# Performance work log

Measured on AMD Instinct MI355X. Metric: run time of the kernel, lower is better.

## Reference

```python
import jax, jax.numpy as jnp
import numpy as np

APREC = 8   # activation fractional bits
PPREC = 8   # parameter fractional bits
IWIDTH = 3  # integer width -> clamp to [-2**IWIDTH, 2**IWIDTH - 1]

QMAX = 2.0 ** IWIDTH - 1.0
QMIN = -(2.0 ** IWIDTH)


def quant(v, prec):
    # round to 2**-prec grid (torch.round and jnp.round both round-half-to-even)
    s = 2.0 ** prec
    return jnp.round(v * s) / s


def round_max(v):
    # the relu-chain in the source is exactly a clamp to [QMIN, QMAX]
    return jnp.clip(v, QMIN, QMAX)


def fixed_point_conv(x, w, b):
    """Quantized 'conv': each elementwise product w[j,m,p,q]*x[b,m,k+p,l+q] is
    rounded to the activation grid and clamped BEFORE summation, then bias added.
    x: [B,Cin,H,W], w: [Cout,Cin,K,K], b: [Cout].
    Loop is over the KxK fixed kernel offsets (25), fully vectorized over B/Cout/Cin/space."""
    w = quant(w, PPREC)
    b = quant(b, PPREC)
    K = w.shape[2]
    Ho = x.shape[2] - K + 1
    Wo = x.shape[3] - K + 1
    out = jnp.zeros((x.shape[0], w.shape[0], Ho, Wo), dtype=x.dtype)
    for p in range(K):
        for q in range(K):
            # [B, Cout, Cin, Ho, Wo]
            prod = x[:, None, :, p:p + Ho, q:q + Wo] * w[None, :, :, p, q, None, None]
            prod = round_max(quant(prod, APREC))
            out = out + prod.sum(axis=2)
    return out + b[None, :, None, None]


def fixed_point_fc(x, w, b):
    # x: [B, in], w: [out, in], b: [out]
    w = round_max(quant(w, PPREC))
    b = round_max(quant(b, PPREC))
    x = round_max(quant(x, APREC))
    out = x @ w.T + b[None, :]
    out = round_max(out)
    return quant(out, APREC)


def max_pool2(x):
    return jax.lax.reduce_window(x, -jnp.inf, jax.lax.max,
                                 (1, 1, 2, 2), (1, 1, 2, 2), 'VALID')


def setup_inputs() -> dict:
    key = jax.random.key(0)
    ks = jax.random.split(key, 9)
    B = 2048
    return {
        'x': jax.random.normal(ks[0], (B, 1, 28, 28), jnp.float32),
        'conv1_w': jax.random.normal(ks[1], (10, 1, 5, 5), jnp.float32) * 0.2,
        'conv1_b': jax.random.normal(ks[2], (10,), jnp.float32) * 0.1,
        'conv2_w': jax.random.normal(ks[3], (20, 10, 5, 5), jnp.float32) * 0.1,
        'conv2_b': jax.random.normal(ks[4], (20,), jnp.float32) * 0.1,
        'fc1_w': jax.random.normal(ks[5], (50, 320), jnp.float32) * 0.05,
        'fc1_b': jax.random.normal(ks[6], (50,), jnp.float32) * 0.05,
        'fc2_w': jax.random.normal(ks[7], (10, 50), jnp.float32) * 0.1,
        'fc2_b': jax.random.normal(ks[8], (10,), jnp.float32) * 0.1,
    }


def reference(x, conv1_w, conv1_b, conv2_w, conv2_b, fc1_w, fc1_b, fc2_w, fc2_b):
    x = quant(x, APREC)
    conv1_input = x
    x = fixed_point_conv(x, conv1_w, conv1_b)          # [B,10,24,24]
    x = quant(x, APREC)
    conv1_output = x
    x = jax.nn.relu(max_pool2(x))                      # [B,10,12,12]
    x = quant(x, APREC)
    conv2_input = x
    x = fixed_point_conv(x, conv2_w, conv2_b)          # [B,20,8,8]
    x = quant(x, APREC)
    conv2_output = x
    # Dropout2d / F.dropout are identity in eval mode
    x = jax.nn.relu(max_pool2(x))                      # [B,20,4,4]
    x = x.reshape(-1, 320)
    x = quant(x, APREC)
    fc1_input = x
    x = fixed_point_fc(x, fc1_w, fc1_b)                # [B,50]
    x = quant(x, APREC)
    fc1_output = x
    x = jax.nn.relu(x)
    x = quant(x, APREC)
    fc2_input = x
    x = fixed_point_fc(x, fc2_w, fc2_b)                # [B,10]
    x = quant(x, APREC)
    fc2_output = x
    logp = jax.nn.log_softmax(x, axis=1)
    return (logp, conv1_input, conv1_output, conv2_input, conv2_output,
            fc1_input, fc1_output, fc2_input, fc2_output)
```

## Files before the change

kernel.cpp:

```cpp
#include <hip/hip_runtime.h>
#include <math.h>


#define NB 2048

#define OFF_LOGP   0
#define OFF_C1IN   (OFF_LOGP  + NB*10)
#define OFF_C1OUT  (OFF_C1IN  + NB*784)
#define OFF_C2IN   (OFF_C1OUT + NB*5760)
#define OFF_C2OUT  (OFF_C2IN  + NB*1440)
#define OFF_FC1IN  (OFF_C2OUT + NB*1280)
#define OFF_FC1OUT (OFF_FC1IN + NB*320)
#define OFF_FC2IN  (OFF_FC1OUT+ NB*50)
#define OFF_FC2OUT (OFF_FC2IN + NB*50)

#define MAGIC_F 12582912.0f

#define WS_WT1 0
#define WS_B1  20480
#define WS_WT2 20544
#define WS_B2  21344
#define WS_CW2 21360
#define WS_CB2 26960
#define WS_CW1 26980
#define WS_CB1 27260

__device__ __forceinline__ float clamp8(float v) {
    return __builtin_amdgcn_fmed3f(v, -8.0f, 7.0f);
}

__global__ __launch_bounds__(256)
void k0_prep(const float* __restrict__ cw1, const float* __restrict__ cb1,
             const float* __restrict__ cw2, const float* __restrict__ cb2,
             const float* __restrict__ fw1, const float* __restrict__ fb1,
             const float* __restrict__ fw2, const float* __restrict__ fb2,
             float* __restrict__ ws)
{
    const int t = threadIdx.x, b = blockIdx.x;
    if (b < 50) {
        const float* src = fw1 + b * 320;
        for (int i = t; i < 320; i += 256)
            ws[WS_WT1 + i * 64 + b] = clamp8(rintf(src[i] * 256.0f) * (1.0f / 256.0f));
    } else if (b == 50) {
        for (int idx = t; idx < 320 * 14; idx += 256) {
            int i = idx / 14, j = 50 + idx % 14;
            ws[WS_WT1 + i * 64 + j] = 0.0f;
        }
        for (int idx = t; idx < 800; idx += 256) {
            int k = idx >> 4, j = idx & 15;
            ws[WS_WT2 + idx] = (j < 10) ? clamp8(rintf(fw2[j * 50 + k] * 256.0f) * (1.0f / 256.0f)) : 0.0f;
        }
        if (t < 64) ws[WS_B1 + t] = (t < 50) ? clamp8(rintf(fb1[t] * 256.0f) * (1.0f / 256.0f)) : 0.0f;
        if (t < 16) ws[WS_B2 + t] = (t < 10) ? clamp8(rintf(fb2[t] * 256.0f) * (1.0f / 256.0f)) : 0.0f;
    } else {
        for (int idx = t; idx < 5600; idx += 256) {
            int cc = idx / 28, col = idx % 28;
            ws[WS_CW2 + idx] = (col < 25) ? rintf(cw2[cc * 25 + col] * 256.0f) : 0.0f;
        }
        if (t < 20) ws[WS_CB2 + t] = rintf(cb2[t] * 256.0f);
        for (int idx = t; idx < 280; idx += 256) {
            int cc = idx / 28, col = idx % 28;
            ws[WS_CW1 + idx] = (col < 25) ? rintf(cw1[cc * 25 + col] * 256.0f) : 0.0f;
        }
        if (t >= 32 && t < 42) ws[WS_CB1 + (t - 32)] = rintf(cb1[t - 32] * 256.0f);
    }
}

__global__ __launch_bounds__(256, 2)
void k12w(const float* __restrict__ x, const float* __restrict__ ws,
          float* __restrict__ out)
{
    __shared__ __align__(16) float s_w1[280];
    __shared__ float s_b1[10];
    __shared__ __align__(16) float s_w2[5600];
    __shared__ float s_b2[20];
    __shared__ __align__(16) float s_x[4][784];
    __shared__ __align__(16) float s_p1[4][1440];

    const int t    = threadIdx.x;
    const int img0 = blockIdx.x * 4;

    {
        const float4* wsrc = (const float4*)(ws + WS_CW2);
        float4* wdst = (float4*)s_w2;
        for (int i = t; i < 1400; i += 256) wdst[i] = wsrc[i];
        if (t < 70) ((float4*)s_w1)[t] = ((const float4*)(ws + WS_CW1))[t];
    }
    if (t >= 70 && t < 80)  s_b1[t - 70] = ws[WS_CB1 + (t - 70)];
    if (t >= 80 && t < 100) s_b2[t - 80] = ws[WS_CB2 + (t - 80)];

    {
        const float* xg = x + (size_t)img0 * 784;
        float* c1in_g = out + OFF_C1IN + (size_t)img0 * 784;
        float* sxf = &s_x[0][0];
        for (int i = t; i < 3136; i += 256) {
            float v = rintf(xg[i] * 256.0f) * (1.0f / 256.0f);
            sxf[i] = v;
            c1in_g[i] = v;
        }
    }
    __syncthreads();

    const int wv  = t >> 6;
    const int L   = t & 63;
    const int img = img0 + wv;
    const float* sx = s_x[wv];
    float*       sp = s_p1[wv];
    float*       sf = s_x[wv];

    if (L < 48) {
        const int i  = L >> 1;
        const int jh = L & 1;

        for (int co = 0; co < 10; co++) {
            asm volatile("" ::: "memory");
            float wreg[28];
            {
                const float* wb = s_w1 + co * 28;
                #pragma unroll
                for (int k = 0; k < 7; k++) {
                    float4 v4 = *(const float4*)(wb + 4 * k);
                    wreg[4*k] = v4.x; wreg[4*k+1] = v4.y; wreg[4*k+2] = v4.z; wreg[4*k+3] = v4.w;
                }
            }
            float acc[12];
            #pragma unroll
            for (int j = 0; j < 12; j++) acc[j] = MAGIC_F;
            #pragma unroll
            for (int p = 0; p < 5; p++) {
                float xr[16];
                const float* row = sx + (i + p) * 28 + 12 * jh;
                #pragma unroll
                for (int k = 0; k < 4; k++) {
                    float4 v4 = *(const float4*)(row + 4 * k);
                    xr[4*k] = v4.x; xr[4*k+1] = v4.y; xr[4*k+2] = v4.z; xr[4*k+3] = v4.w;
                }
                #pragma unroll
                for (int q = 0; q < 5; q++) {
                    float w = wreg[p * 5 + q];
                    #pragma unroll
                    for (int j = 0; j < 12; j++)
                        acc[j] = fmaf(xr[q + j], w, acc[j]);
                }
            }
            const float C = MAGIC_F - s_b1[co];
            float v[12];
            #pragma unroll
            for (int j = 0; j < 12; j++) v[j] = (acc[j] - C) * (1.0f / 256.0f);

            float* gdst = out + OFF_C1OUT + (size_t)img * 5760 + co * 576 + i * 24 + 12 * jh;
            #pragma unroll
            for (int k = 0; k < 3; k++) {
                float4 st = { v[4*k], v[4*k+1], v[4*k+2], v[4*k+3] };
                *(float4*)(gdst + 4 * k) = st;
            }

            float m[6];
            #pragma unroll
            for (int j2 = 0; j2 < 6; j2++) m[j2] = fmaxf(v[2*j2], v[2*j2+1]);
            float pm[6];
            #pragma unroll
            for (int j2 = 0; j2 < 6; j2++) pm[j2] = __shfl_xor(m[j2], 2);

            if ((i & 1) == 0) {
                float pr[6];
                #pragma unroll
                for (int j2 = 0; j2 < 6; j2++)
                    pr[j2] = fmaxf(fmaxf(m[j2], pm[j2]), 0.0f);
                const int o = co * 144 + (i >> 1) * 12 + 6 * jh;
                float* g = out + OFF_C2IN + (size_t)img * 1440 + o;
                #pragma unroll
                for (int k = 0; k < 3; k++) {
                    float2 st = { pr[2*k], pr[2*k+1] };
                    *(float2*)(g + 2 * k) = st;
                    *(float2*)(sp + o + 2 * k) = st;
                }
            }
        }
    }

    const int ch = L & 1;
    const int i2 = (L >> 1) & 7;
    for (int g = 0; g < 5; g++) {
        asm volatile("" ::: "memory");
        const int co = 4 * g + (L >> 4);

        float acc[8];
        #pragma unroll
        for (int j = 0; j < 8; j++) acc[j] = MAGIC_F;

        #pragma unroll
        for (int cc = 0; cc < 5; cc++) {
            const int ci = ch * 5 + cc;
            float wreg[28];
            {
                const float* wb = s_w2 + (co * 10 + ci) * 28;
                #pragma unroll
                for (int k = 0; k < 7; k++) {
                    float4 v4 = *(const float4*)(wb + 4 * k);
                    wreg[4*k] = v4.x; wreg[4*k+1] = v4.y; wreg[4*k+2] = v4.z; wreg[4*k+3] = v4.w;
                }
            }
            const float* xb = sp + ci * 144;
            #pragma unroll
            for (int p = 0; p < 5; p++) {
                const float* row = xb + (i2 + p) * 12;
                float4 a4 = *(const float4*)(row);
                float4 b4 = *(const float4*)(row + 4);
                float4 c4 = *(const float4*)(row + 8);
                float xr[12] = { a4.x, a4.y, a4.z, a4.w, b4.x, b4.y, b4.z, b4.w,
                                 c4.x, c4.y, c4.z, c4.w };
                #pragma unroll
                for (int q = 0; q < 5; q++) {
                    float w = wreg[p * 5 + q];
                    #pragma unroll
                    for (int j = 0; j < 8; j++)
                        acc[j] = fmaf(xr[q + j], w, acc[j]);
                }
            }
        }

        float s[8];
        #pragma unroll
        for (int j = 0; j < 8; j++) s[j] = acc[j] - MAGIC_F;
        #pragma unroll
        for (int j = 0; j < 8; j++) s[j] += __shfl_xor(s[j], 1);

        const float b2 = s_b2[co];
        float v[8];
        #pragma unroll
        for (int j = 0; j < 8; j++) v[j] = (s[j] + b2) * (1.0f / 256.0f);

        float m[4], pm[4];
        #pragma unroll
        for (int c = 0; c < 4; c++) m[c] = fmaxf(v[2*c], v[2*c+1]);
        #pragma unroll
        for (int c = 0; c < 4; c++) pm[c] = __shfl_xor(m[c], 2);

        if (ch == 0) {
            float4 st0 = { v[0], v[1], v[2], v[3] };
            float4 st1 = { v[4], v[5], v[6], v[7] };
            float* cdst = out + OFF_C2OUT + (size_t)img * 1280 + co * 64 + i2 * 8;
            *(float4*)(cdst)     = st0;
            *(float4*)(cdst + 4) = st1;

            if ((i2 & 1) == 0) {
                float4 pr = { fmaxf(fmaxf(m[0], pm[0]), 0.0f),
                              fmaxf(fmaxf(m[1], pm[1]), 0.0f),
                              fmaxf(fmaxf(m[2], pm[2]), 0.0f),
                              fmaxf(fmaxf(m[3], pm[3]), 0.0f) };
                const int o = co * 16 + (i2 >> 1) * 4;
                *(float4*)(out + OFF_FC1IN + (size_t)img * 320 + o) = pr;
                float4 prc = { clamp8(pr.x), clamp8(pr.y), clamp8(pr.z), clamp8(pr.w) };
                *(float4*)(sf + o) = prc;
            }
        }
    }

    float acc = ws[WS_B1 + L];
    #pragma unroll 8
    for (int k = 0; k < 320; k++)
        acc = fmaf(sf[k], ws[WS_WT1 + k * 64 + L], acc);
    float o1 = rintf(clamp8(acc) * 256.0f) * (1.0f / 256.0f);
    float r1 = fmaxf(o1, 0.0f);
    if (L < 50) {
        out[OFF_FC1OUT + (size_t)img * 50 + L] = o1;
        out[OFF_FC2IN  + (size_t)img * 50 + L] = r1;
    }
    float yc = clamp8(r1);

    float acc2 = ws[WS_B2 + (L & 15)];
    #pragma unroll 10
    for (int k = 0; k < 50; k++) {
        float yk = __shfl(yc, k);
        acc2 = fmaf(yk, ws[WS_WT2 + k * 16 + (L & 15)], acc2);
    }
    float o2 = rintf(clamp8(acc2) * 256.0f) * (1.0f / 256.0f);
    if (L < 10) out[OFF_FC2OUT + (size_t)img * 10 + L] = o2;

    float vmx = (L < 10) ? o2 : -3.0e38f;
    #pragma unroll
    for (int d = 1; d < 16; d <<= 1)
        vmx = fmaxf(vmx, __shfl_xor(vmx, d, 16));
    float e = (L < 10) ? expf(o2 - vmx) : 0.0f;
    #pragma unroll
    for (int d = 1; d < 16; d <<= 1)
        e += __shfl_xor(e, d, 16);
    float lse = vmx + logf(e);
    if (L < 10) out[OFF_LOGP + (size_t)img * 10 + L] = o2 - lse;
}

extern "C" void kernel_launch(void* const* d_in, const int* in_sizes, int n_in,
                              void* d_out, int out_size, void* d_ws, size_t ws_size,
                              hipStream_t stream) {
    const float* x   = (const float*)d_in[0];
    const float* cw1 = (const float*)d_in[1];
    const float* cb1 = (const float*)d_in[2];
    const float* cw2 = (const float*)d_in[3];
    const float* cb2 = (const float*)d_in[4];
    const float* fw1 = (const float*)d_in[5];
    const float* fb1 = (const float*)d_in[6];
    const float* fw2 = (const float*)d_in[7];
    const float* fb2 = (const float*)d_in[8];
    float* o  = (float*)d_out;
    float* ws = (float*)d_ws;

    k0_prep<<<52, 256, 0, stream>>>(cw1, cb1, cw2, cb2, fw1, fb1, fw2, fb2, ws);
    k12w   <<<NB / 4, 256, 0, stream>>>(x, ws, o);
}
```

Baseline: 163.9 us.

## Process one image per 128-thread block and split conv channels across waves

```diff
diff --git a/kernel.cpp b/kernel.cpp
--- a/kernel.cpp
+++ b/kernel.cpp
@@ -66,57 +66,39 @@
     }
 }
 
-__global__ __launch_bounds__(256, 2)
+__global__ __launch_bounds__(128, 4)
 void k12w(const float* __restrict__ x, const float* __restrict__ ws,
           float* __restrict__ out)
 {
-    __shared__ __align__(16) float s_w1[280];
-    __shared__ float s_b1[10];
-    __shared__ __align__(16) float s_w2[5600];
-    __shared__ float s_b2[20];
-    __shared__ __align__(16) float s_x[4][784];
-    __shared__ __align__(16) float s_p1[4][1440];
-
-    const int t    = threadIdx.x;
-    const int img0 = blockIdx.x * 4;
-
-    {
-        const float4* wsrc = (const float4*)(ws + WS_CW2);
-        float4* wdst = (float4*)s_w2;
-        for (int i = t; i < 1400; i += 256) wdst[i] = wsrc[i];
-        if (t < 70) ((float4*)s_w1)[t] = ((const float4*)(ws + WS_CW1))[t];
-    }
-    if (t >= 70 && t < 80)  s_b1[t - 70] = ws[WS_CB1 + (t - 70)];
-    if (t >= 80 && t < 100) s_b2[t - 80] = ws[WS_CB2 + (t - 80)];
-
-    {
-        const float* xg = x + (size_t)img0 * 784;
-        float* c1in_g = out + OFF_C1IN + (size_t)img0 * 784;
-        float* sxf = &s_x[0][0];
-        for (int i = t; i < 3136; i += 256) {
-            float v = rintf(xg[i] * 256.0f) * (1.0f / 256.0f);
-            sxf[i] = v;
-            c1in_g[i] = v;
-        }
-    }
-    __syncthreads();
-
+    __shared__ __align__(16) float s_x[784];
+    __shared__ __align__(16) float s_p1[1440];
+
+    const int t   = threadIdx.x;
+    const int img = blockIdx.x;
     const int wv  = t >> 6;
     const int L   = t & 63;
-    const int img = img0 + wv;
-    const float* sx = s_x[wv];
-    float*       sp = s_p1[wv];
-    float*       sf = s_x[wv];
+
+    {
+        const float* xg = x + (size_t)img * 784;
+        float* c1in_g = out + OFF_C1IN + (size_t)img * 784;
+        for (int i = t; i < 784; i += 128) {
+            float v = rintf(xg[i] * 256.0f) * (1.0f / 256.0f);
+            s_x[i] = v;
+            c1in_g[i] = v;
+        }
+    }
+    __syncthreads();
 
     if (L < 48) {
         const int i  = L >> 1;
         const int jh = L & 1;
 
-        for (int co = 0; co < 10; co++) {
+        for (int c5 = 0; c5 < 5; c5++) {
             asm volatile("" ::: "memory");
+            const int co = wv * 5 + c5;
             float wreg[28];
             {
-                const float* wb = s_w1 + co * 28;
+                const float* wb = ws + WS_CW1 + co * 28;
                 #pragma unroll
                 for (int k = 0; k < 7; k++) {
                     float4 v4 = *(const float4*)(wb + 4 * k);
@@ -129,7 +111,7 @@
             #pragma unroll
             for (int p = 0; p < 5; p++) {
                 float xr[16];
-                const float* row = sx + (i + p) * 28 + 12 * jh;
+                const float* row = s_x + (i + p) * 28 + 12 * jh;
                 #pragma unroll
                 for (int k = 0; k < 4; k++) {
                     float4 v4 = *(const float4*)(row + 4 * k);
@@ -143,7 +125,7 @@
                         acc[j] = fmaf(xr[q + j], w, acc[j]);
                 }
             }
-            const float C = MAGIC_F - s_b1[co];
+            const float C = MAGIC_F - ws[WS_CB1 + co];
             float v[12];
             #pragma unroll
             for (int j = 0; j < 12; j++) v[j] = (acc[j] - C) * (1.0f / 256.0f);
@@ -173,18 +155,17 @@
                 for (int k = 0; k < 3; k++) {
                     float2 st = { pr[2*k], pr[2*k+1] };
                     *(float2*)(g + 2 * k) = st;
-                    *(float2*)(sp + o + 2 * k) = st;
-                }
-            }
-        }
-    }
-
-    const int ch = L & 1;
-    const int i2 = (L >> 1) & 7;
-    for (int g = 0; g < 5; g++) {
-        asm volatile("" ::: "memory");
-        const int co = 4 * g + (L >> 4);
-
+                    *(float2*)(s_p1 + o + 2 * k) = st;
+                }
+            }
+        }
+    }
+    __syncthreads();
+
+    const int ch = t & 1;
+    const int i2 = (t >> 1) & 7;
+
+    auto conv2_body = [&](int co) {
         float acc[8];
         #pragma unroll
         for (int j = 0; j < 8; j++) acc[j] = MAGIC_F;
@@ -194,14 +175,14 @@
             const int ci = ch * 5 + cc;
             float wreg[28];
             {
-                const float* wb = s_w2 + (co * 10 + ci) * 28;
+                const float* wb = ws + WS_CW2 + (co * 10 + ci) * 28;
                 #pragma unroll
                 for (int k = 0; k < 7; k++) {
                     float4 v4 = *(const float4*)(wb + 4 * k);
                     wreg[4*k] = v4.x; wreg[4*k+1] = v4.y; wreg[4*k+2] = v4.z; wreg[4*k+3] = v4.w;
                 }
             }
-            const float* xb = sp + ci * 144;
+            const float* xb = s_p1 + ci * 144;
             #pragma unroll
             for (int p = 0; p < 5; p++) {
                 const float* row = xb + (i2 + p) * 12;
@@ -226,7 +207,7 @@
         #pragma unroll
         for (int j = 0; j < 8; j++) s[j] += __shfl_xor(s[j], 1);
 
-        const float b2 = s_b2[co];
+        const float b2 = ws[WS_CB2 + co];
         float v[8];
         #pragma unroll
         for (int j = 0; j < 8; j++) v[j] = (s[j] + b2) * (1.0f / 256.0f);
@@ -252,42 +233,55 @@
                 const int o = co * 16 + (i2 >> 1) * 4;
                 *(float4*)(out + OFF_FC1IN + (size_t)img * 320 + o) = pr;
                 float4 prc = { clamp8(pr.x), clamp8(pr.y), clamp8(pr.z), clamp8(pr.w) };
-                *(float4*)(sf + o) = prc;
-            }
-        }
-    }
-
-    float acc = ws[WS_B1 + L];
-    #pragma unroll 8
-    for (int k = 0; k < 320; k++)
-        acc = fmaf(sf[k], ws[WS_WT1 + k * 64 + L], acc);
-    float o1 = rintf(clamp8(acc) * 256.0f) * (1.0f / 256.0f);
-    float r1 = fmaxf(o1, 0.0f);
-    if (L < 50) {
-        out[OFF_FC1OUT + (size_t)img * 50 + L] = o1;
-        out[OFF_FC2IN  + (size_t)img * 50 + L] = r1;
-    }
-    float yc = clamp8(r1);
-
-    float acc2 = ws[WS_B2 + (L & 15)];
-    #pragma unroll 10
-    for (int k = 0; k < 50; k++) {
-        float yk = __shfl(yc, k);
-        acc2 = fmaf(yk, ws[WS_WT2 + k * 16 + (L & 15)], acc2);
-    }
-    float o2 = rintf(clamp8(acc2) * 256.0f) * (1.0f / 256.0f);
-    if (L < 10) out[OFF_FC2OUT + (size_t)img * 10 + L] = o2;
-
-    float vmx = (L < 10) ? o2 : -3.0e38f;
-    #pragma unroll
-    for (int d = 1; d < 16; d <<= 1)
-        vmx = fmaxf(vmx, __shfl_xor(vmx, d, 16));
-    float e = (L < 10) ? expf(o2 - vmx) : 0.0f;
-    #pragma unroll
-    for (int d = 1; d < 16; d <<= 1)
-        e += __shfl_xor(e, d, 16);
-    float lse = vmx + logf(e);
-    if (L < 10) out[OFF_LOGP + (size_t)img * 10 + L] = o2 - lse;
+                *(float4*)(s_x + o) = prc;
+            }
+        }
+    };
+
+    for (int g = 0; g < 2; g++) {
+        asm volatile("" ::: "memory");
+        conv2_body(g * 8 + (t >> 4));
+    }
+    if (L < 32) {
+        asm volatile("" ::: "memory");
+        conv2_body(16 + wv * 2 + ((t & 31) >> 4));
+    }
+    __syncthreads();
+
+    if (wv == 0) {
+        const float* sf = s_x;
+        float acc = ws[WS_B1 + L];
+        #pragma unroll 8
+        for (int k = 0; k < 320; k++)
+            acc = fmaf(sf[k], ws[WS_WT1 + k * 64 + L], acc);
+        float o1 = rintf(clamp8(acc) * 256.0f) * (1.0f / 256.0f);
+        float r1 = fmaxf(o1, 0.0f);
+        if (L < 50) {
+            out[OFF_FC1OUT + (size_t)img * 50 + L] = o1;
+            out[OFF_FC2IN  + (size_t)img * 50 + L] = r1;
+        }
+        float yc = clamp8(r1);
+
+        float acc2 = ws[WS_B2 + (L & 15)];
+        #pragma unroll 10
+        for (int k = 0; k < 50; k++) {
+            float yk = __shfl(yc, k);
+            acc2 = fmaf(yk, ws[WS_WT2 + k * 16 + (L & 15)], acc2);
+        }
+        float o2 = rintf(clamp8(acc2) * 256.0f) * (1.0f / 256.0f);
+        if (L < 10) out[OFF_FC2OUT + (size_t)img * 10 + L] = o2;
+
+        float vmx = (L < 10) ? o2 : -3.0e38f;
+        #pragma unroll
+        for (int d = 1; d < 16; d <<= 1)
+            vmx = fmaxf(vmx, __shfl_xor(vmx, d, 16));
+        float e = (L < 10) ? expf(o2 - vmx) : 0.0f;
+        #pragma unroll
+        for (int d = 1; d < 16; d <<= 1)
+            e += __shfl_xor(e, d, 16);
+        float lse = vmx + logf(e);
+        if (L < 10) out[OFF_LOGP + (size_t)img * 10 + L] = o2 - lse;
+    }
 }
 
 extern "C" void kernel_launch(void* const* d_in, const int* in_sizes, int n_in,
@@ -306,5 +300,5 @@
     float* ws = (float*)d_ws;
 
     k0_prep<<<52, 256, 0, stream>>>(cw1, cb1, cw2, cb2, fw1, fb1, fw2, fb2, ws);
-    k12w   <<<NB / 4, 256, 0, stream>>>(x, ws, o);
+    k12w   <<<NB, 128, 0, stream>>>(x, ws, o);
 }
```

Result: faster. 159.7 us (-2.5%).
